# Performance work log

Hardware: AMD Instinct MI355X
Metric: run time of the kernel (lower is better)

## Reference

```python
import jax, jax.numpy as jnp
import numpy as np

B, C, H, W = 16, 192, 48, 48
D_STATE, DT_RANK, D_INNER, K = 16, 16, 288, 4


def setup_inputs() -> dict:
    key = jax.random.key(0)
    ks = jax.random.split(key, 8)
    g = lambda k, shape, scale: jax.random.normal(k, shape, jnp.float32) * scale
    # S4D-real style init: A_log = log(1..N)
    A_log = jnp.tile(jnp.log(jnp.arange(1.0, D_STATE + 1.0, dtype=jnp.float32)), (K, D_INNER, 1))
    return {
        "x": jax.random.normal(ks[0], (B, C, H, W), jnp.float32),
        "W_in": g(ks[1], (C, 2 * D_INNER), C ** -0.5),
        "conv_w": g(ks[2], (D_INNER, 1, 3, 3), 1.0 / 3.0),
        "conv_b": jnp.zeros((D_INNER,), jnp.float32),
        "x_proj_w": g(ks[3], (K, DT_RANK + 2 * D_STATE, D_INNER), D_INNER ** -0.5),
        "dt_w": g(ks[4], (K, D_INNER, DT_RANK), DT_RANK ** -0.5),
        "dt_b": g(ks[5], (K, D_INNER), 0.5) - 4.0,
        "A_log": A_log,
        "Ds": jnp.ones((K, D_INNER), jnp.float32),
        "ln_g": jnp.ones((D_INNER,), jnp.float32),
        "ln_b": jnp.zeros((D_INNER,), jnp.float32),
        "W_out": g(ks[6], (D_INNER, C), D_INNER ** -0.5),
        "bn_g": jnp.ones((C,), jnp.float32),
        "bn_b": jnp.zeros((C,), jnp.float32),
    }


def reference(x, W_in, conv_w, conv_b, x_proj_w, dt_w, dt_b, A_log, Ds,
              ln_g, ln_b, W_out, bn_g, bn_b):
    b, c, h, w = x.shape
    L = h * w
    # MambaBlock: NCHW -> NHWC, SS2D(v2), NHWC -> NCHW, BatchNorm2d
    xhwc = jnp.transpose(x, (0, 2, 3, 1))                        # (B,H,W,C)
    xz = xhwc @ W_in                                             # (B,H,W,2*Di)
    xc, z = jnp.split(xz, 2, axis=-1)
    # depthwise 3x3 conv + SiLU
    xc = jnp.transpose(xc, (0, 3, 1, 2))                         # (B,Di,H,W)
    xc = jax.lax.conv_general_dilated(
        xc, conv_w, (1, 1), ((1, 1), (1, 1)),
        dimension_numbers=('NCHW', 'OIHW', 'NCHW'),
        feature_group_count=D_INNER)
    xc = jax.nn.silu(xc + conv_b[None, :, None, None])
    # cross-scan: 4 directions (row-major, col-major, + reversals)
    x_hw = xc.reshape(b, D_INNER, L)
    x_wh = jnp.transpose(xc, (0, 1, 3, 2)).reshape(b, D_INNER, L)
    xs = jnp.stack([x_hw, x_wh], axis=1)
    xs = jnp.concatenate([xs, jnp.flip(xs, axis=-1)], axis=1)    # (B,K,Di,L)
    # input-dependent dt, B, C
    x_dbl = jnp.einsum('bkdl,kcd->bkcl', xs, x_proj_w)
    dts, Bmat, Cmat = jnp.split(x_dbl, [DT_RANK, DT_RANK + D_STATE], axis=2)
    dt = jnp.einsum('bkrl,kdr->bkdl', dts, dt_w)
    dt = jax.nn.softplus(dt + dt_b[None, :, :, None])            # (B,K,Di,L)
    A = -jnp.exp(A_log)                                          # (K,Di,N)
    # selective scan along L (sequential recurrence)
    us = jnp.transpose(xs, (3, 0, 1, 2))                         # (L,B,K,Di)
    dts_t = jnp.transpose(dt, (3, 0, 1, 2))
    Bs_t = jnp.transpose(Bmat, (3, 0, 1, 2))                     # (L,B,K,N)
    Cs_t = jnp.transpose(Cmat, (3, 0, 1, 2))

    def step(hst, inp):
        u_t, d_t, B_t, C_t = inp
        dA = jnp.exp(d_t[..., None] * A)                         # (B,K,Di,N)
        hst = dA * hst + (d_t * u_t)[..., None] * B_t[:, :, None, :]
        y_t = jnp.sum(hst * C_t[:, :, None, :], axis=-1)         # (B,K,Di)
        return hst, y_t

    h0 = jnp.zeros((b, K, D_INNER, D_STATE), xs.dtype)
    _, ys = jax.lax.scan(step, h0, (us, dts_t, Bs_t, Cs_t))
    ys = jnp.transpose(ys, (1, 2, 3, 0))                         # (B,K,Di,L)
    ys = ys + Ds[None, :, :, None] * xs                          # skip (D) term
    # cross-merge: undo flips / transpose and sum the 4 directions
    y = ys[:, 0] + jnp.flip(ys[:, 2], axis=-1)
    y_wh = ys[:, 1] + jnp.flip(ys[:, 3], axis=-1)                # col-major order
    y = y + jnp.transpose(y_wh.reshape(b, D_INNER, w, h), (0, 1, 3, 2)).reshape(b, D_INNER, L)
    y = jnp.transpose(y.reshape(b, D_INNER, h, w), (0, 2, 3, 1))  # (B,H,W,Di)
    # out_norm (LayerNorm over channels), gating, out projection
    mu = jnp.mean(y, axis=-1, keepdims=True)
    var = jnp.var(y, axis=-1, keepdims=True)
    y = (y - mu) * jax.lax.rsqrt(var + 1e-5) * ln_g + ln_b
    y = y * jax.nn.silu(z)
    out = jnp.transpose(y @ W_out, (0, 3, 1, 2))                 # (B,C,H,W)
    # BatchNorm2d (training-mode batch statistics)
    m = jnp.mean(out, axis=(0, 2, 3), keepdims=True)
    v = jnp.var(out, axis=(0, 2, 3), keepdims=True)
    out = (out - m) * jax.lax.rsqrt(v + 1e-5) * bn_g[None, :, None, None] + bn_b[None, :, None, None]
    return out
```

## Files before the change

kernel.cpp:

```cpp
#include <hip/hip_runtime.h>
#include <hip/hip_fp16.h>
#include <math.h>

#define BB 16
#define CC 192
#define LL 2304
#define DI 288
#define NS 16

typedef float f32x4 __attribute__((ext_vector_type(4)));
typedef short bf16x8 __attribute__((ext_vector_type(8)));

__device__ __forceinline__ short f2b(float f) {
  union { float f; unsigned u; } x; x.f = f;
  unsigned r = x.u + 0x7FFF + ((x.u >> 16) & 1);
  return (short)(r >> 16);
}

__device__ __forceinline__ float softplus_f(float v) {
  return v > 15.f ? v : __logf(1.f + __expf(v));
}

__device__ __forceinline__ int pos_of(int k, int t) {
  int tt = (k >= 2) ? (2303 - t) : t;
  if (k & 1) return (tt % 48) * 48 + tt / 48;
  return tt;
}
__device__ __forceinline__ int invpos(int k, int l) {
  int tt = (k & 1) ? (l % 48) * 48 + l / 48 : l;
  return (k >= 2) ? (2303 - tt) : tt;
}

__device__ __forceinline__ void pow_table(float E, float* P) {
  float p2 = E * E, p4 = p2 * p2, p8 = p4 * p4;
  P[0] = E;       P[1] = p2;      P[2] = p2 * E;  P[3] = p4;
  P[4] = p4 * E;  P[5] = p4 * p2; P[6] = p4 * P[2]; P[7] = p8;
  P[8] = p8 * E;  P[9] = p8 * p2; P[10] = p8 * P[2]; P[11] = p8 * p4;
  P[12] = p8 * P[4]; P[13] = p8 * P[5]; P[14] = p8 * P[6]; P[15] = p8 * p8;
}

__global__ __launch_bounds__(256) void k_wprep(const float* __restrict__ Win,
                                               const float* __restrict__ xpw,
                                               const float* __restrict__ Wout,
                                               short* __restrict__ winb,
                                               short* __restrict__ xpwb,
                                               short* __restrict__ woutb) {
  int i = blockIdx.x * 256 + threadIdx.x;
  if (i < 110592) {
    int j = i / 192, c = i % 192;
    winb[i] = f2b(Win[(size_t)c * 576 + j]);
  } else if (i < 165888) {
    int t = i - 110592;
    xpwb[t] = f2b(xpw[t]);
  } else {
    int t = i - 165888;
    int j = t / 288, d = t % 288;
    woutb[t] = f2b(Wout[(size_t)d * 192 + j]);
  }
}

__global__ __launch_bounds__(256) void k_check(const float* __restrict__ alog,
                                               int* __restrict__ flag) {
  __shared__ int ok;
  if (threadIdx.x == 0) ok = 1;
  __syncthreads();
  int bad = 0;
  for (int i = threadIdx.x; i < 4 * DI * NS; i += 256) {
    int n = i & 15;
    float t = __logf((float)(n + 1));
    if (fabsf(alog[i] - t) > 1e-5f) bad = 1;
  }
  if (bad) atomicAnd(&ok, 0);
  __syncthreads();
  if (threadIdx.x == 0) *flag = ok;
}

__global__ __launch_bounds__(256) void g_inproj(const float* __restrict__ x,
                                                const short* __restrict__ winb,
                                                float* __restrict__ xc,
                                                float* __restrict__ z) {
  __shared__ short As[64 * 200];
  __shared__ short Bs[48 * 200];
  int nt = blockIdx.x % 12, mt = blockIdx.x / 12;
  int b = mt / 36, l0 = (mt % 36) * 64;
  int j0 = nt * 48;
  int tid = threadIdx.x;
  for (int i = tid; i < 3072; i += 256) {
    int c = i >> 4, lq = i & 15;
    float4 v = *(const float4*)&x[((size_t)b * CC + c) * LL + l0 + lq * 4];
    As[(lq * 4 + 0) * 200 + c] = f2b(v.x);
    As[(lq * 4 + 1) * 200 + c] = f2b(v.y);
    As[(lq * 4 + 2) * 200 + c] = f2b(v.z);
    As[(lq * 4 + 3) * 200 + c] = f2b(v.w);
  }
  for (int i = tid; i < 1152; i += 256) {
    int n = i / 24, kq = i % 24;
    *(bf16x8*)&Bs[n * 200 + kq * 8] =
        *(const bf16x8*)&winb[(size_t)(j0 + n) * 192 + kq * 8];
  }
  __syncthreads();
  int w = tid >> 6, lane = tid & 63;
  int ln = lane & 15, q8 = (lane >> 4) * 8;
  int m0 = w * 16;
  f32x4 acc0 = {0.f, 0.f, 0.f, 0.f}, acc1 = acc0, acc2 = acc0;
#pragma unroll
  for (int kt = 0; kt < 6; ++kt) {
    bf16x8 a = *(bf16x8*)&As[(m0 + ln) * 200 + kt * 32 + q8];
    bf16x8 b0 = *(bf16x8*)&Bs[(0 * 16 + ln) * 200 + kt * 32 + q8];
    bf16x8 b1 = *(bf16x8*)&Bs[(1 * 16 + ln) * 200 + kt * 32 + q8];
    bf16x8 b2 = *(bf16x8*)&Bs[(2 * 16 + ln) * 200 + kt * 32 + q8];
    acc0 = __builtin_amdgcn_mfma_f32_16x16x32_bf16(a, b0, acc0, 0, 0, 0);
    acc1 = __builtin_amdgcn_mfma_f32_16x16x32_bf16(a, b1, acc1, 0, 0, 0);
    acc2 = __builtin_amdgcn_mfma_f32_16x16x32_bf16(a, b2, acc2, 0, 0, 0);
  }
  int mrow = m0 + (lane >> 4) * 4;
  if (nt < 6) {
#pragma unroll
    for (int r = 0; r < 4; ++r) {
      size_t rb = ((size_t)b * LL + l0 + mrow + r) * DI + j0;
      xc[rb + 0 * 16 + ln] = acc0[r];
      xc[rb + 1 * 16 + ln] = acc1[r];
      xc[rb + 2 * 16 + ln] = acc2[r];
    }
  } else {
    __syncthreads();
    float* Zs = (float*)As;
#pragma unroll
    for (int r = 0; r < 4; ++r) {
      int lm = mrow + r - 0;
      Zs[(0 * 16 + ln) * 66 + lm] = acc0[r];
      Zs[(1 * 16 + ln) * 66 + lm] = acc1[r];
      Zs[(2 * 16 + ln) * 66 + lm] = acc2[r];
    }
    __syncthreads();
    int j2base = j0 - DI;
    for (int i = tid; i < 768; i += 256) {
      int j = i >> 4, lq = i & 15;
      float4 v = make_float4(Zs[j * 66 + lq * 4 + 0], Zs[j * 66 + lq * 4 + 1],
                             Zs[j * 66 + lq * 4 + 2], Zs[j * 66 + lq * 4 + 3]);
      *(float4*)&z[((size_t)b * DI + j2base + j) * LL + l0 + lq * 4] = v;
    }
  }
}

__global__ __launch_bounds__(288) void k_conv2(const float* __restrict__ xc,
                                               const float* __restrict__ cw,
                                               const float* __restrict__ cb,
                                               float* __restrict__ co) {
  int b = blockIdx.x / 48, h = blockIdx.x % 48;
  int d = threadIdx.x;
  float wv[9];
#pragma unroll
  for (int j = 0; j < 9; ++j) wv[j] = cw[d * 9 + j];
  float bias = cb[d];
  bool hm = h > 0, hp = h < 47;
  const float* row0 = xc + ((size_t)b * LL + (h - 1) * 48) * DI + d;
  const float* row1 = xc + ((size_t)b * LL + h * 48) * DI + d;
  const float* row2 = xc + ((size_t)b * LL + (h + 1) * 48) * DI + d;
  float* op = co + ((size_t)b * LL + h * 48) * DI + d;
  float a0 = 0.f, a1 = 0.f, a2 = 0.f;
  float b0, b1, b2, c0, c1, c2;
  b0 = hm ? row0[0] : 0.f;
  b1 = row1[0];
  b2 = hp ? row2[0] : 0.f;
  for (int w = 0; w < 48; ++w) {
    if (w < 47) {
      int off = (w + 1) * DI;
      c0 = hm ? row0[off] : 0.f;
      c1 = row1[off];
      c2 = hp ? row2[off] : 0.f;
    } else {
      c0 = 0.f; c1 = 0.f; c2 = 0.f;
    }
    float acc = bias;
    acc = fmaf(a0, wv[0], acc); acc = fmaf(b0, wv[1], acc); acc = fmaf(c0, wv[2], acc);
    acc = fmaf(a1, wv[3], acc); acc = fmaf(b1, wv[4], acc); acc = fmaf(c1, wv[5], acc);
    acc = fmaf(a2, wv[6], acc); acc = fmaf(b2, wv[7], acc); acc = fmaf(c2, wv[8], acc);
    acc = acc / (1.f + __expf(-acc));
    op[w * DI] = acc;
    a0 = b0; a1 = b1; a2 = b2;
    b0 = c0; b1 = c1; b2 = c2;
  }
}

__global__ __launch_bounds__(256) void g_xdbl(const float* __restrict__ co,
                                              const short* __restrict__ xpwb,
                                              float* __restrict__ xd) {
  __shared__ short As[64 * 296];
  __shared__ short Bs[48 * 296];
  int nt = blockIdx.x % 4, mt = blockIdx.x / 4;
  int b = mt / 36, l0 = (mt % 36) * 64;
  int j0 = nt * 48;
  int tid = threadIdx.x;
  for (int i = tid; i < 2304; i += 256) {
    int m = i / 36, kq = i % 36;
    const float* src = &co[((size_t)b * LL + l0 + m) * DI + kq * 8];
    float4 f0 = *(const float4*)src;
    float4 f1 = *(const float4*)(src + 4);
    bf16x8 v;
    v[0] = f2b(f0.x); v[1] = f2b(f0.y); v[2] = f2b(f0.z); v[3] = f2b(f0.w);
    v[4] = f2b(f1.x); v[5] = f2b(f1.y); v[6] = f2b(f1.z); v[7] = f2b(f1.w);
    *(bf16x8*)&As[m * 296 + kq * 8] = v;
  }
  for (int i = tid; i < 1728; i += 256) {
    int n = i / 36, kq = i % 36;
    *(bf16x8*)&Bs[n * 296 + kq * 8] =
        *(const bf16x8*)&xpwb[(size_t)(j0 + n) * 288 + kq * 8];
  }
  __syncthreads();
  int w = tid >> 6, lane = tid & 63;
  int ln = lane & 15, q8 = (lane >> 4) * 8;
  int m0 = w * 16;
  f32x4 acc0 = {0.f, 0.f, 0.f, 0.f}, acc1 = acc0, acc2 = acc0;
#pragma unroll
  for (int kt = 0; kt < 9; ++kt) {
    bf16x8 a = *(bf16x8*)&As[(m0 + ln) * 296 + kt * 32 + q8];
    bf16x8 b0 = *(bf16x8*)&Bs[(0 * 16 + ln) * 296 + kt * 32 + q8];
    bf16x8 b1 = *(bf16x8*)&Bs[(1 * 16 + ln) * 296 + kt * 32 + q8];
    bf16x8 b2 = *(bf16x8*)&Bs[(2 * 16 + ln) * 296 + kt * 32 + q8];
    acc0 = __builtin_amdgcn_mfma_f32_16x16x32_bf16(a, b0, acc0, 0, 0, 0);
    acc1 = __builtin_amdgcn_mfma_f32_16x16x32_bf16(a, b1, acc1, 0, 0, 0);
    acc2 = __builtin_amdgcn_mfma_f32_16x16x32_bf16(a, b2, acc2, 0, 0, 0);
  }
  int mrow = m0 + (lane >> 4) * 4;
#pragma unroll
  for (int r = 0; r < 4; ++r) {
    size_t rb = (((size_t)b * 4 + nt) * LL + l0 + mrow + r) * 48;
    xd[rb + 0 * 16 + ln] = acc0[r];
    xd[rb + 1 * 16 + ln] = acc1[r];
    xd[rb + 2 * 16 + ln] = acc2[r];
  }
}

__global__ __launch_bounds__(288) void g_dt(const float* __restrict__ xd,
                                            const float* __restrict__ dtw,
                                            const float* __restrict__ dtb,
                                            __half* __restrict__ dth) {
  int blk = blockIdx.x;
  int lc = blk % 72, bk = blk / 72;
  int k = bk & 3;
  int d = threadIdx.x;
  float w_dt[16];
#pragma unroll
  for (int r4 = 0; r4 < 4; ++r4) {
    float4 t4 = *(const float4*)&dtw[((size_t)k * DI + d) * 16 + r4 * 4];
    w_dt[r4 * 4 + 0] = t4.x; w_dt[r4 * 4 + 1] = t4.y;
    w_dt[r4 * 4 + 2] = t4.z; w_dt[r4 * 4 + 3] = t4.w;
  }
  float bias = dtb[k * DI + d];
  const float* __restrict__ xb = xd + (size_t)bk * LL * 48;
  __half* __restrict__ Eb = dth + (size_t)bk * LL * DI;
#pragma unroll 2
  for (int j = 0; j < 32; ++j) {
    int l = lc * 32 + j;
    const float* __restrict__ xr = xb + (size_t)l * 48;
    float4 v0 = *(const float4*)(xr + 0);
    float4 v1 = *(const float4*)(xr + 4);
    float4 v2 = *(const float4*)(xr + 8);
    float4 v3 = *(const float4*)(xr + 12);
    float a0 = fmaf(v0.x, w_dt[0], bias);
    float a1 = v0.y * w_dt[1];
    float a2 = v0.z * w_dt[2];
    float a3 = v0.w * w_dt[3];
    a0 = fmaf(v1.x, w_dt[4], a0); a1 = fmaf(v1.y, w_dt[5], a1);
    a2 = fmaf(v1.z, w_dt[6], a2); a3 = fmaf(v1.w, w_dt[7], a3);
    a0 = fmaf(v2.x, w_dt[8], a0); a1 = fmaf(v2.y, w_dt[9], a1);
    a2 = fmaf(v2.z, w_dt[10], a2); a3 = fmaf(v2.w, w_dt[11], a3);
    a0 = fmaf(v3.x, w_dt[12], a0); a1 = fmaf(v3.y, w_dt[13], a1);
    a2 = fmaf(v3.z, w_dt[14], a2); a3 = fmaf(v3.w, w_dt[15], a3);
    float v = (a0 + a1) + (a2 + a3);
    float dt = v > 15.f ? v : __logf(1.f + __expf(v));
    int t = invpos(k, l);
    Eb[(size_t)t * DI + d] = __float2half(dt);
  }
}

template <int SCHT, bool USE_E>
__global__ __launch_bounds__(288) void k_pass1(const float* __restrict__ co,
                                               const float* __restrict__ xd,
                                               const float* __restrict__ dtw,
                                               const float* __restrict__ dtb,
                                               const float* __restrict__ alog,
                                               const int* __restrict__ flag,
                                               const __half* __restrict__ dth,
                                               float* __restrict__ HL,
                                               float* __restrict__ Sd) {
  constexpr int TCHT = LL / SCHT;
  int blk = blockIdx.x;
  int s = blk % SCHT, k = (blk / SCHT) & 3, b = blk / (SCHT * 4);
  int d = threadIdx.x;
  float w_dt[16];
  float bias = 0.f;
  if constexpr (!USE_E) {
#pragma unroll
    for (int r4 = 0; r4 < 4; ++r4) {
      float4 t4 = *(const float4*)&dtw[((size_t)k * DI + d) * 16 + r4 * 4];
      w_dt[r4 * 4 + 0] = t4.x; w_dt[r4 * 4 + 1] = t4.y;
      w_dt[r4 * 4 + 2] = t4.z; w_dt[r4 * 4 + 3] = t4.w;
    }
    bias = dtb[k * DI + d];
  }
  float h[16];
#pragma unroll
  for (int n = 0; n < 16; ++n) h[n] = 0.f;
  const float* __restrict__ xb = xd + ((size_t)b * 4 + k) * LL * 48;
  const float* __restrict__ cb_ = co + (size_t)b * LL * DI;
  const __half* __restrict__ Eb = dth + ((size_t)b * 4 + k) * LL * DI;
  int fast = *flag;
  size_t base = ((size_t)((b * 4 + k) * SCHT + s) * DI + d) * 16;
  size_t sbase = ((size_t)((b * 4 + k) * SCHT + s) * DI + d);
  float S = 0.f;
  if (fast) {
    for (int i = 0; i < TCHT; ++i) {
      int t = s * TCHT + i;
      int l = __builtin_amdgcn_readfirstlane(pos_of(k, t));
      const float* __restrict__ xr = xb + (size_t)l * 48;
      float4 q0 = *(const float4*)(xr + 16);
      float4 q1 = *(const float4*)(xr + 20);
      float4 q2 = *(const float4*)(xr + 24);
      float4 q3 = *(const float4*)(xr + 28);
      float u = cb_[(size_t)l * DI + d];
      float E, dt;
      if constexpr (USE_E) {
        dt = __half2float(Eb[(size_t)t * DI + d]);
        E = __expf(-dt);
      } else {
        float4 v0 = *(const float4*)(xr + 0);
        float4 v1 = *(const float4*)(xr + 4);
        float4 v2 = *(const float4*)(xr + 8);
        float4 v3 = *(const float4*)(xr + 12);
        float a0 = fmaf(v0.x, w_dt[0], bias), a1 = v0.y * w_dt[1];
        float a2 = v0.z * w_dt[2], a3 = v0.w * w_dt[3];
        a0 = fmaf(v1.x, w_dt[4], a0); a1 = fmaf(v1.y, w_dt[5], a1);
        a2 = fmaf(v1.z, w_dt[6], a2); a3 = fmaf(v1.w, w_dt[7], a3);
        a0 = fmaf(v2.x, w_dt[8], a0); a1 = fmaf(v2.y, w_dt[9], a1);
        a2 = fmaf(v2.z, w_dt[10], a2); a3 = fmaf(v2.w, w_dt[11], a3);
        a0 = fmaf(v3.x, w_dt[12], a0); a1 = fmaf(v3.y, w_dt[13], a1);
        a2 = fmaf(v3.z, w_dt[14], a2); a3 = fmaf(v3.w, w_dt[15], a3);
        float v = (a0 + a1) + (a2 + a3);
        float ev = __expf(v);
        E = __builtin_amdgcn_rcpf(1.f + ev);
        dt = v > 15.f ? v : __logf(1.f + ev);
      }
      float xv = dt * u;
      S += dt;
      float P[16];
      pow_table(E, P);
      float Bv[16] = {q0.x, q0.y, q0.z, q0.w, q1.x, q1.y, q1.z, q1.w,
                      q2.x, q2.y, q2.z, q2.w, q3.x, q3.y, q3.z, q3.w};
#pragma unroll
      for (int n = 0; n < 16; ++n) h[n] = fmaf(P[n], h[n], xv * Bv[n]);
    }
  } else {
    float A[16];
#pragma unroll
    for (int n = 0; n < 16; ++n) A[n] = -__expf(alog[((size_t)k * DI + d) * 16 + n]);
    for (int i = 0; i < TCHT; ++i) {
      int t = s * TCHT + i;
      int l = __builtin_amdgcn_readfirstlane(pos_of(k, t));
      const float* __restrict__ xr = xb + (size_t)l * 48;
      float4 q0 = *(const float4*)(xr + 16);
      float4 q1 = *(const float4*)(xr + 20);
      float4 q2 = *(const float4*)(xr + 24);
      float4 q3 = *(const float4*)(xr + 28);
      float u = cb_[(size_t)l * DI + d];
      float dt;
      if constexpr (USE_E) {
        dt = __half2float(Eb[(size_t)t * DI + d]);
      } else {
        float a0 = bias, a1 = 0.f, a2 = 0.f, a3 = 0.f;
#pragma unroll
        for (int r = 0; r < 4; ++r) {
          a0 = fmaf(xr[r * 4 + 0], w_dt[r * 4 + 0], a0);
          a1 = fmaf(xr[r * 4 + 1], w_dt[r * 4 + 1], a1);
          a2 = fmaf(xr[r * 4 + 2], w_dt[r * 4 + 2], a2);
          a3 = fmaf(xr[r * 4 + 3], w_dt[r * 4 + 3], a3);
        }
        dt = softplus_f((a0 + a1) + (a2 + a3));
      }
      float xv = dt * u;
      S += dt;
      float Bv[16] = {q0.x, q0.y, q0.z, q0.w, q1.x, q1.y, q1.z, q1.w,
                      q2.x, q2.y, q2.z, q2.w, q3.x, q3.y, q3.z, q3.w};
#pragma unroll
      for (int n = 0; n < 16; ++n) {
        float dA = __expf(dt * A[n]);
        h[n] = fmaf(dA, h[n], xv * Bv[n]);
      }
    }
  }
  Sd[sbase] = S;
#pragma unroll
  for (int n = 0; n < 16; ++n) HL[base + n] = h[n];
}

template <int SCHT>
__global__ __launch_bounds__(256) void k_stitch(float* __restrict__ HL,
                                                const float* __restrict__ Sd,
                                                const float* __restrict__ alog,
                                                const int* __restrict__ flag) {
  int idx = blockIdx.x * 256 + threadIdx.x;
  if (idx >= 64 * DI) return;
  int d = idx % DI, bk = idx / DI;
  int k = bk & 3;
  int fast = *flag;
  float A[16];
  if (!fast) {
#pragma unroll
    for (int n = 0; n < 16; ++n) A[n] = -__expf(alog[((size_t)k * DI + d) * 16 + n]);
  }
  float h[16];
#pragma unroll
  for (int n = 0; n < 16; ++n) h[n] = 0.f;
  for (int s = 0; s < SCHT; ++s) {
    size_t base = ((size_t)(bk * SCHT + s) * DI + d) * 16;
    float S = Sd[(size_t)(bk * SCHT + s) * DI + d];
    float Q[16];
    if (fast) {
      pow_table(__expf(-S), Q);
    } else {
#pragma unroll
      for (int n = 0; n < 16; ++n) Q[n] = __expf(A[n] * S);
    }
#pragma unroll
    for (int n = 0; n < 16; ++n) {
      float hl = HL[base + n];
      HL[base + n] = h[n];
      h[n] = fmaf(Q[n], h[n], hl);
    }
  }
}

template <int SCHT, bool USE_E>
__global__ __launch_bounds__(288) void k_pass2(const float* __restrict__ co,
                                               const float* __restrict__ xd,
                                               const float* __restrict__ dtw,
                                               const float* __restrict__ dtb,
                                               const float* __restrict__ alog,
                                               const int* __restrict__ flag,
                                               const __half* __restrict__ dth,
                                               const float* __restrict__ Hin,
                                               float* __restrict__ ym) {
  constexpr int TCHT = LL / SCHT;
  int blk = blockIdx.x;
  int s = blk % SCHT, k = (blk / SCHT) & 3, b = blk / (SCHT * 4);
  int d = threadIdx.x;
  float w_dt[16];
  float bias = 0.f;
  if constexpr (!USE_E) {
#pragma unroll
    for (int r4 = 0; r4 < 4; ++r4) {
      float4 t4 = *(const float4*)&dtw[((size_t)k * DI + d) * 16 + r4 * 4];
      w_dt[r4 * 4 + 0] = t4.x; w_dt[r4 * 4 + 1] = t4.y;
      w_dt[r4 * 4 + 2] = t4.z; w_dt[r4 * 4 + 3] = t4.w;
    }
    bias = dtb[k * DI + d];
  }
  size_t base = ((size_t)((b * 4 + k) * SCHT + s) * DI + d) * 16;
  float h[16];
#pragma unroll
  for (int n = 0; n < 16; ++n) h[n] = Hin[base + n];
  const float* __restrict__ xb = xd + ((size_t)b * 4 + k) * LL * 48;
  const float* __restrict__ cb_ = co + (size_t)b * LL * DI;
  const __half* __restrict__ Eb = dth + ((size_t)b * 4 + k) * LL * DI;
  float* __restrict__ yb = ym + (size_t)b * LL * DI;
  int fast = *flag;
  if (fast) {
    for (int i = 0; i < TCHT; ++i) {
      int t = s * TCHT + i;
      int l = __builtin_amdgcn_readfirstlane(pos_of(k, t));
      const float* __restrict__ xr = xb + (size_t)l * 48;
      float4 q0 = *(const float4*)(xr + 16);
      float4 q1 = *(const float4*)(xr + 20);
      float4 q2 = *(const float4*)(xr + 24);
      float4 q3 = *(const float4*)(xr + 28);
      float4 c0 = *(const float4*)(xr + 32);
      float4 c1 = *(const float4*)(xr + 36);
      float4 c2 = *(const float4*)(xr + 40);
      float4 c3 = *(const float4*)(xr + 44);
      float u = cb_[(size_t)l * DI + d];
      float E, dt;
      if constexpr (USE_E) {
        dt = __half2float(Eb[(size_t)t * DI + d]);
        E = __expf(-dt);
      } else {
        float4 v0 = *(const float4*)(xr + 0);
        float4 v1 = *(const float4*)(xr + 4);
        float4 v2 = *(const float4*)(xr + 8);
        float4 v3 = *(const float4*)(xr + 12);
        float a0 = fmaf(v0.x, w_dt[0], bias), a1 = v0.y * w_dt[1];
        float a2 = v0.z * w_dt[2], a3 = v0.w * w_dt[3];
        a0 = fmaf(v1.x, w_dt[4], a0); a1 = fmaf(v1.y, w_dt[5], a1);
        a2 = fmaf(v1.z, w_dt[6], a2); a3 = fmaf(v1.w, w_dt[7], a3);
        a0 = fmaf(v2.x, w_dt[8], a0); a1 = fmaf(v2.y, w_dt[9], a1);
        a2 = fmaf(v2.z, w_dt[10], a2); a3 = fmaf(v2.w, w_dt[11], a3);
        a0 = fmaf(v3.x, w_dt[12], a0); a1 = fmaf(v3.y, w_dt[13], a1);
        a2 = fmaf(v3.z, w_dt[14], a2); a3 = fmaf(v3.w, w_dt[15], a3);
        float v = (a0 + a1) + (a2 + a3);
        float ev = __expf(v);
        E = __builtin_amdgcn_rcpf(1.f + ev);
        dt = v > 15.f ? v : __logf(1.f + ev);
      }
      float xv = dt * u;
      float P[16];
      pow_table(E, P);
      float Bv[16] = {q0.x, q0.y, q0.z, q0.w, q1.x, q1.y, q1.z, q1.w,
                      q2.x, q2.y, q2.z, q2.w, q3.x, q3.y, q3.z, q3.w};
      float Cv[16] = {c0.x, c0.y, c0.z, c0.w, c1.x, c1.y, c1.z, c1.w,
                      c2.x, c2.y, c2.z, c2.w, c3.x, c3.y, c3.z, c3.w};
      float y0 = 0.f, y1 = 0.f, y2 = 0.f, y3 = 0.f;
#pragma unroll
      for (int n = 0; n < 16; n += 4) {
        h[n + 0] = fmaf(P[n + 0], h[n + 0], xv * Bv[n + 0]);
        h[n + 1] = fmaf(P[n + 1], h[n + 1], xv * Bv[n + 1]);
        h[n + 2] = fmaf(P[n + 2], h[n + 2], xv * Bv[n + 2]);
        h[n + 3] = fmaf(P[n + 3], h[n + 3], xv * Bv[n + 3]);
        y0 = fmaf(h[n + 0], Cv[n + 0], y0);
        y1 = fmaf(h[n + 1], Cv[n + 1], y1);
        y2 = fmaf(h[n + 2], Cv[n + 2], y2);
        y3 = fmaf(h[n + 3], Cv[n + 3], y3);
      }
      atomicAdd(&yb[(size_t)l * DI + d], (y0 + y1) + (y2 + y3));
    }
  } else {
    float A[16];
#pragma unroll
    for (int n = 0; n < 16; ++n) A[n] = -__expf(alog[((size_t)k * DI + d) * 16 + n]);
    for (int i = 0; i < TCHT; ++i) {
      int t = s * TCHT + i;
      int l = __builtin_amdgcn_readfirstlane(pos_of(k, t));
      const float* __restrict__ xr = xb + (size_t)l * 48;
      float4 q0 = *(const float4*)(xr + 16);
      float4 q1 = *(const float4*)(xr + 20);
      float4 q2 = *(const float4*)(xr + 24);
      float4 q3 = *(const float4*)(xr + 28);
      float4 c0 = *(const float4*)(xr + 32);
      float4 c1 = *(const float4*)(xr + 36);
      float4 c2 = *(const float4*)(xr + 40);
      float4 c3 = *(const float4*)(xr + 44);
      float u = cb_[(size_t)l * DI + d];
      float dt;
      if constexpr (USE_E) {
        dt = __half2float(Eb[(size_t)t * DI + d]);
      } else {
        float a0 = bias, a1 = 0.f, a2 = 0.f, a3 = 0.f;
#pragma unroll
        for (int r = 0; r < 4; ++r) {
          a0 = fmaf(xr[r * 4 + 0], w_dt[r * 4 + 0], a0);
          a1 = fmaf(xr[r * 4 + 1], w_dt[r * 4 + 1], a1);
          a2 = fmaf(xr[r * 4 + 2], w_dt[r * 4 + 2], a2);
          a3 = fmaf(xr[r * 4 + 3], w_dt[r * 4 + 3], a3);
        }
        dt = softplus_f((a0 + a1) + (a2 + a3));
      }
      float xv = dt * u;
      float Bv[16] = {q0.x, q0.y, q0.z, q0.w, q1.x, q1.y, q1.z, q1.w,
                      q2.x, q2.y, q2.z, q2.w, q3.x, q3.y, q3.z, q3.w};
      float Cv[16] = {c0.x, c0.y, c0.z, c0.w, c1.x, c1.y, c1.z, c1.w,
                      c2.x, c2.y, c2.z, c2.w, c3.x, c3.y, c3.z, c3.w};
      float y = 0.f;
#pragma unroll
      for (int n = 0; n < 16; ++n) {
        float dA = __expf(dt * A[n]);
        h[n] = fmaf(dA, h[n], xv * Bv[n]);
        y = fmaf(h[n], Cv[n], y);
      }
      atomicAdd(&yb[(size_t)l * DI + d], y);
    }
  }
}

__global__ __launch_bounds__(256) void k_ln(const float* __restrict__ ym,
                                            const float* __restrict__ co,
                                            const float* __restrict__ z,
                                            const float* __restrict__ Ds,
                                            const float* __restrict__ lng,
                                            const float* __restrict__ lnb,
                                            float* __restrict__ Yl) {
  __shared__ float As[DI * 33];
  __shared__ float red[512];
  __shared__ float mus[32], rss[32];
  int b = blockIdx.x / 72;
  int l0 = (blockIdx.x % 72) * 32;
  for (int i = threadIdx.x; i < DI * 32; i += 256) {
    int l = i / DI, d = i % DI;
    float sds = Ds[d] + Ds[DI + d] + Ds[2 * DI + d] + Ds[3 * DI + d];
    size_t off = ((size_t)b * LL + l0 + l) * DI + d;
    As[d * 33 + l] = ym[off] + sds * co[off];
  }
  __syncthreads();
  int l = threadIdx.x & 31;
  int p = threadIdx.x >> 5;
  float s1 = 0.f, s2 = 0.f;
  for (int d = p; d < DI; d += 8) {
    float v = As[d * 33 + l];
    s1 += v; s2 += v * v;
  }
  red[p * 32 + l] = s1;
  red[256 + p * 32 + l] = s2;
  __syncthreads();
  if (threadIdx.x < 32) {
    float su = 0.f, sq = 0.f;
#pragma unroll
    for (int q = 0; q < 8; ++q) { su += red[q * 32 + l]; sq += red[256 + q * 32 + l]; }
    float mu = su * (1.f / 288.f);
    float var = sq * (1.f / 288.f) - mu * mu;
    mus[l] = mu;
    rss[l] = rsqrtf(var + 1e-5f);
  }
  __syncthreads();
  {
    float mu = mus[l], rs = rss[l];
    for (int d = p; d < DI; d += 8) {
      float v = (As[d * 33 + l] - mu) * rs * lng[d] + lnb[d];
      float zv = z[((size_t)b * DI + d) * LL + l0 + l];
      v *= zv / (1.f + __expf(-zv));
      As[d * 33 + l] = v;
    }
  }
  __syncthreads();
  for (int i = threadIdx.x; i < DI * 32; i += 256) {
    int ll = i / DI, d = i % DI;
    Yl[((size_t)b * LL + l0 + ll) * DI + d] = As[d * 33 + ll];
  }
}

__global__ __launch_bounds__(256) void g_outproj(const float* __restrict__ Yl,
                                                 const short* __restrict__ woutb,
                                                 float* __restrict__ out,
                                                 float* __restrict__ bnsum,
                                                 float* __restrict__ bnsq) {
  __shared__ short As[64 * 296];
  __shared__ short Bs[48 * 296];
  int nt = blockIdx.x % 4, mt = blockIdx.x / 4;
  int b = mt / 36, l0 = (mt % 36) * 64;
  int j0 = nt * 48;
  int tid = threadIdx.x;
  for (int i = tid; i < 2304; i += 256) {
    int m = i / 36, kq = i % 36;
    const float* src = &Yl[((size_t)b * LL + l0 + m) * DI + kq * 8];
    float4 f0 = *(const float4*)src;
    float4 f1 = *(const float4*)(src + 4);
    bf16x8 v;
    v[0] = f2b(f0.x); v[1] = f2b(f0.y); v[2] = f2b(f0.z); v[3] = f2b(f0.w);
    v[4] = f2b(f1.x); v[5] = f2b(f1.y); v[6] = f2b(f1.z); v[7] = f2b(f1.w);
    *(bf16x8*)&As[m * 296 + kq * 8] = v;
  }
  for (int i = tid; i < 1728; i += 256) {
    int n = i / 36, kq = i % 36;
    *(bf16x8*)&Bs[n * 296 + kq * 8] =
        *(const bf16x8*)&woutb[(size_t)(j0 + n) * 288 + kq * 8];
  }
  __syncthreads();
  int w = tid >> 6, lane = tid & 63;
  int ln = lane & 15, q8 = (lane >> 4) * 8;
  int m0 = w * 16;
  f32x4 acc0 = {0.f, 0.f, 0.f, 0.f}, acc1 = acc0, acc2 = acc0;
#pragma unroll
  for (int kt = 0; kt < 9; ++kt) {
    bf16x8 a = *(bf16x8*)&As[(m0 + ln) * 296 + kt * 32 + q8];
    bf16x8 b0 = *(bf16x8*)&Bs[(0 * 16 + ln) * 296 + kt * 32 + q8];
    bf16x8 b1 = *(bf16x8*)&Bs[(1 * 16 + ln) * 296 + kt * 32 + q8];
    bf16x8 b2 = *(bf16x8*)&Bs[(2 * 16 + ln) * 296 + kt * 32 + q8];
    acc0 = __builtin_amdgcn_mfma_f32_16x16x32_bf16(a, b0, acc0, 0, 0, 0);
    acc1 = __builtin_amdgcn_mfma_f32_16x16x32_bf16(a, b1, acc1, 0, 0, 0);
    acc2 = __builtin_amdgcn_mfma_f32_16x16x32_bf16(a, b2, acc2, 0, 0, 0);
  }
  __syncthreads();
  float* Zs = (float*)As;
  int lm = m0 + (lane >> 4) * 4;
#pragma unroll
  for (int r = 0; r < 4; ++r) {
    Zs[(0 * 16 + ln) * 66 + lm + r] = acc0[r];
    Zs[(1 * 16 + ln) * 66 + lm + r] = acc1[r];
    Zs[(2 * 16 + ln) * 66 + lm + r] = acc2[r];
  }
  __syncthreads();
  for (int i = tid; i < 768; i += 256) {
    int j = i >> 4, lq = i & 15;
    float4 v = make_float4(Zs[j * 66 + lq * 4 + 0], Zs[j * 66 + lq * 4 + 1],
                           Zs[j * 66 + lq * 4 + 2], Zs[j * 66 + lq * 4 + 3]);
    *(float4*)&out[((size_t)b * CC + j0 + j) * LL + l0 + lq * 4] = v;
  }
  if (tid < 48) {
    float s1 = 0.f, s2 = 0.f;
#pragma unroll 8
    for (int l = 0; l < 64; ++l) {
      float v = Zs[tid * 66 + l];
      s1 += v; s2 += v * v;
    }
    atomicAdd(&bnsum[j0 + tid], s1);
    atomicAdd(&bnsq[j0 + tid], s2);
  }
}

__global__ __launch_bounds__(256) void k_bnfin(float* __restrict__ out,
                                               const float* __restrict__ bnsum,
                                               const float* __restrict__ bnsq,
                                               const float* __restrict__ bg,
                                               const float* __restrict__ bb) {
  int idx = blockIdx.x * 256 + threadIdx.x;
  int c = (idx / LL) % CC;
  float mean = bnsum[c] * (1.f / 36864.f);
  float var = bnsq[c] * (1.f / 36864.f) - mean * mean;
  float sc = bg[c] * rsqrtf(var + 1e-5f);
  out[idx] = (out[idx] - mean) * sc + bb[c];
}

extern "C" void kernel_launch(void* const* d_in, const int* in_sizes, int n_in,
                              void* d_out, int out_size, void* d_ws, size_t ws_size,
                              hipStream_t stream) {
  (void)in_sizes; (void)n_in; (void)out_size;
  const float* x    = (const float*)d_in[0];
  const float* Win  = (const float*)d_in[1];
  const float* cw   = (const float*)d_in[2];
  const float* cbb  = (const float*)d_in[3];
  const float* xpw  = (const float*)d_in[4];
  const float* dtw  = (const float*)d_in[5];
  const float* dtb  = (const float*)d_in[6];
  const float* alog = (const float*)d_in[7];
  const float* Ds   = (const float*)d_in[8];
  const float* lng  = (const float*)d_in[9];
  const float* lnb  = (const float*)d_in[10];
  const float* Wout = (const float*)d_in[11];
  const float* bg   = (const float*)d_in[12];
  const float* bb   = (const float*)d_in[13];
  float* out = (float*)d_out;

  const size_t NXC = 10616832, NXD = 7077888;
  const size_t NWB = 110592;
  const size_t NE  = 42467328;
  const size_t REH = NE / 2;
  auto hlN = [](int sch) { return (size_t)64 * sch * DI * 16; };
  auto sdN = [](int sch) { return (size_t)64 * sch * DI; };
  auto needE = [&](int sch) {
    return (3 * NXC + NWB + NXD + REH + hlN(sch) + sdN(sch) + 1024) * 4;
  };
  auto needN = [&](int sch) {
    return (3 * NXC + NWB + NXD + hlN(sch) + sdN(sch) + 1024) * 4;
  };
  bool useE; int sch;
  if (ws_size >= needE(32))      { useE = true;  sch = 32; }
  else if (ws_size >= needE(16)) { useE = true;  sch = 16; }
  else if (ws_size >= needN(32)) { useE = false; sch = 32; }
  else                           { useE = false; sch = 16; }

  float* ws = (float*)d_ws;
  float* z   = ws;
  float* A1  = z + NXC;
  float* co  = A1 + NXC;
  float* wbF = co + NXC;
  float* xd  = wbF + NWB;
  float* R   = xd + NXD;
  short* winb  = (short*)wbF;
  short* xpwb  = (short*)(wbF + 55296);
  short* woutb = (short*)(wbF + 55296 + 27648);
  float *xc, *ym, *tail;
  __half* dth = nullptr;
  if (useE) {
    xc = R;
    ym = A1;
    dth = (__half*)R;
    tail = R + REH;
  } else {
    xc = A1; ym = A1;
    tail = R;
  }
  float* HL = tail;
  float* Sd = HL + hlN(sch);
  float* bnsum = Sd + sdN(sch);
  float* bnsq  = bnsum + 192;
  int*   flag  = (int*)(bnsq + 192);
  float* Yl = xd;

  k_wprep<<<864, 256, 0, stream>>>(Win, xpw, Wout, winb, xpwb, woutb);
  k_check<<<1, 256, 0, stream>>>(alog, flag);
  g_inproj<<<6912, 256, 0, stream>>>(x, winb, xc, z);
  k_conv2<<<768, 288, 0, stream>>>(xc, cw, cbb, co);
  hipMemsetAsync(ym, 0, NXC * 4, stream);
  hipMemsetAsync(bnsum, 0, 2 * 192 * 4, stream);
  g_xdbl<<<2304, 256, 0, stream>>>(co, xpwb, xd);
  if (useE) g_dt<<<4608, 288, 0, stream>>>(xd, dtw, dtb, dth);
  if (useE && sch == 32) {
    k_pass1<32, true><<<2048, 288, 0, stream>>>(co, xd, dtw, dtb, alog, flag, dth, HL, Sd);
    k_stitch<32><<<72, 256, 0, stream>>>(HL, Sd, alog, flag);
    k_pass2<32, true><<<2048, 288, 0, stream>>>(co, xd, dtw, dtb, alog, flag, dth, HL, ym);
  } else if (useE) {
    k_pass1<16, true><<<1024, 288, 0, stream>>>(co, xd, dtw, dtb, alog, flag, dth, HL, Sd);
    k_stitch<16><<<72, 256, 0, stream>>>(HL, Sd, alog, flag);
    k_pass2<16, true><<<1024, 288, 0, stream>>>(co, xd, dtw, dtb, alog, flag, dth, HL, ym);
  } else if (sch == 32) {
    k_pass1<32, false><<<2048, 288, 0, stream>>>(co, xd, dtw, dtb, alog, flag, dth, HL, Sd);
    k_stitch<32><<<72, 256, 0, stream>>>(HL, Sd, alog, flag);
    k_pass2<32, false><<<2048, 288, 0, stream>>>(co, xd, dtw, dtb, alog, flag, dth, HL, ym);
  } else {
    k_pass1<16, false><<<1024, 288, 0, stream>>>(co, xd, dtw, dtb, alog, flag, dth, HL, Sd);
    k_stitch<16><<<72, 256, 0, stream>>>(HL, Sd, alog, flag);
    k_pass2<16, false><<<1024, 288, 0, stream>>>(co, xd, dtw, dtb, alog, flag, dth, HL, ym);
  }
  k_ln<<<1152, 256, 0, stream>>>(ym, co, z, Ds, lng, lnb, Yl);
  g_outproj<<<2304, 256, 0, stream>>>(Yl, woutb, out, bnsum, bnsq);
  k_bnfin<<<27648, 256, 0, stream>>>(out, bnsum, bnsq, bg, bb);
}
```

Measured before the change: 706.4 us.

## Stage B/C scan rows in double-buffered LDS and prefetch next-step inputs

In the USE_E fast path of both scan passes, each block now cooperatively loads the B (and C) vectors for groups of 18 timesteps into a double-buffered shared-memory tile, prefetching the next group while the current one is processed. Per-step u and dt values are also software-prefetched one step ahead in registers. This replaces the per-thread broadcast global loads on the serial critical path with LDS reads and hides global latency. In exchange it adds block-wide barriers per group and extra LDS traffic, and it assumes TCHT is a multiple of 18.

```diff
diff --git a/kernel.cpp b/kernel.cpp
--- a/kernel.cpp
+++ b/kernel.cpp
@@ -286,9 +286,12 @@
                                                float* __restrict__ HL,
                                                float* __restrict__ Sd) {
   constexpr int TCHT = LL / SCHT;
+  constexpr int G = 18;
+  __shared__ float ro[2][G * 16];
   int blk = blockIdx.x;
   int s = blk % SCHT, k = (blk / SCHT) & 3, b = blk / (SCHT * 4);
   int d = threadIdx.x;
+  int tid = threadIdx.x;
   float w_dt[16];
   float bias = 0.f;
   if constexpr (!USE_E) {
@@ -310,7 +313,52 @@
   size_t base = ((size_t)((b * 4 + k) * SCHT + s) * DI + d) * 16;
   size_t sbase = ((size_t)((b * 4 + k) * SCHT + s) * DI + d);
   float S = 0.f;
-  if (fast) {
+  if (fast && USE_E) {
+    int t0 = s * TCHT, tend = t0 + TCHT;
+    {
+      int i = tid >> 4, j = tid & 15;
+      int lg = pos_of(k, t0 + i);
+      ro[0][tid] = xb[(size_t)lg * 48 + 16 + j];
+    }
+    int lc = __builtin_amdgcn_readfirstlane(pos_of(k, t0));
+    float u = cb_[(size_t)lc * DI + d];
+    __half dh = Eb[(size_t)t0 * DI + d];
+    __syncthreads();
+    for (int g = 0; g < TCHT / G; ++g) {
+      int buf = g & 1;
+      if (g + 1 < TCHT / G) {
+        int i = tid >> 4, j = tid & 15;
+        int lg = pos_of(k, t0 + (g + 1) * G + i);
+        ro[buf ^ 1][tid] = xb[(size_t)lg * 48 + 16 + j];
+      }
+      for (int il = 0; il < G; ++il) {
+        int t = t0 + g * G + il;
+        float un = u; __half dhn = dh;
+        if (t + 1 < tend) {
+          int ln_ = __builtin_amdgcn_readfirstlane(pos_of(k, t + 1));
+          un = cb_[(size_t)ln_ * DI + d];
+          dhn = Eb[(size_t)(t + 1) * DI + d];
+        }
+        float dt = __half2float(dh);
+        float E = __expf(-dt);
+        float xv = dt * u;
+        S += dt;
+        float P[16];
+        pow_table(E, P);
+        const float* rp = &ro[buf][il * 16];
+        float4 r0 = *(const float4*)(rp + 0);
+        float4 r1 = *(const float4*)(rp + 4);
+        float4 r2 = *(const float4*)(rp + 8);
+        float4 r3 = *(const float4*)(rp + 12);
+        float Bv[16] = {r0.x, r0.y, r0.z, r0.w, r1.x, r1.y, r1.z, r1.w,
+                        r2.x, r2.y, r2.z, r2.w, r3.x, r3.y, r3.z, r3.w};
+#pragma unroll
+        for (int n = 0; n < 16; ++n) h[n] = fmaf(P[n], h[n], xv * Bv[n]);
+        u = un; dh = dhn;
+      }
+      __syncthreads();
+    }
+  } else if (fast) {
     for (int i = 0; i < TCHT; ++i) {
       int t = s * TCHT + i;
       int l = __builtin_amdgcn_readfirstlane(pos_of(k, t));
@@ -320,28 +368,22 @@
       float4 q2 = *(const float4*)(xr + 24);
       float4 q3 = *(const float4*)(xr + 28);
       float u = cb_[(size_t)l * DI + d];
-      float E, dt;
-      if constexpr (USE_E) {
-        dt = __half2float(Eb[(size_t)t * DI + d]);
-        E = __expf(-dt);
-      } else {
-        float4 v0 = *(const float4*)(xr + 0);
-        float4 v1 = *(const float4*)(xr + 4);
-        float4 v2 = *(const float4*)(xr + 8);
-        float4 v3 = *(const float4*)(xr + 12);
-        float a0 = fmaf(v0.x, w_dt[0], bias), a1 = v0.y * w_dt[1];
-        float a2 = v0.z * w_dt[2], a3 = v0.w * w_dt[3];
-        a0 = fmaf(v1.x, w_dt[4], a0); a1 = fmaf(v1.y, w_dt[5], a1);
-        a2 = fmaf(v1.z, w_dt[6], a2); a3 = fmaf(v1.w, w_dt[7], a3);
-        a0 = fmaf(v2.x, w_dt[8], a0); a1 = fmaf(v2.y, w_dt[9], a1);
-        a2 = fmaf(v2.z, w_dt[10], a2); a3 = fmaf(v2.w, w_dt[11], a3);
-        a0 = fmaf(v3.x, w_dt[12], a0); a1 = fmaf(v3.y, w_dt[13], a1);
-        a2 = fmaf(v3.z, w_dt[14], a2); a3 = fmaf(v3.w, w_dt[15], a3);
-        float v = (a0 + a1) + (a2 + a3);
-        float ev = __expf(v);
-        E = __builtin_amdgcn_rcpf(1.f + ev);
-        dt = v > 15.f ? v : __logf(1.f + ev);
-      }
+      float4 v0 = *(const float4*)(xr + 0);
+      float4 v1 = *(const float4*)(xr + 4);
+      float4 v2 = *(const float4*)(xr + 8);
+      float4 v3 = *(const float4*)(xr + 12);
+      float a0 = fmaf(v0.x, w_dt[0], bias), a1 = v0.y * w_dt[1];
+      float a2 = v0.z * w_dt[2], a3 = v0.w * w_dt[3];
+      a0 = fmaf(v1.x, w_dt[4], a0); a1 = fmaf(v1.y, w_dt[5], a1);
+      a2 = fmaf(v1.z, w_dt[6], a2); a3 = fmaf(v1.w, w_dt[7], a3);
+      a0 = fmaf(v2.x, w_dt[8], a0); a1 = fmaf(v2.y, w_dt[9], a1);
+      a2 = fmaf(v2.z, w_dt[10], a2); a3 = fmaf(v2.w, w_dt[11], a3);
+      a0 = fmaf(v3.x, w_dt[12], a0); a1 = fmaf(v3.y, w_dt[13], a1);
+      a2 = fmaf(v3.z, w_dt[14], a2); a3 = fmaf(v3.w, w_dt[15], a3);
+      float v = (a0 + a1) + (a2 + a3);
+      float ev = __expf(v);
+      float E = __builtin_amdgcn_rcpf(1.f + ev);
+      float dt = v > 15.f ? v : __logf(1.f + ev);
       float xv = dt * u;
       S += dt;
       float P[16];
@@ -442,9 +484,12 @@
                                                const float* __restrict__ Hin,
                                                float* __restrict__ ym) {
   constexpr int TCHT = LL / SCHT;
+  constexpr int G = 18;
+  __shared__ float ro[2][G * 32];
   int blk = blockIdx.x;
   int s = blk % SCHT, k = (blk / SCHT) & 3, b = blk / (SCHT * 4);
   int d = threadIdx.x;
+  int tid = threadIdx.x;
   float w_dt[16];
   float bias = 0.f;
   if constexpr (!USE_E) {
@@ -465,7 +510,75 @@
   const __half* __restrict__ Eb = dth + ((size_t)b * 4 + k) * LL * DI;
   float* __restrict__ yb = ym + (size_t)b * LL * DI;
   int fast = *flag;
-  if (fast) {
+  if (fast && USE_E) {
+    int t0 = s * TCHT, tend = t0 + TCHT;
+    {
+      int f0 = tid, i = f0 >> 5, j = f0 & 31;
+      int lg = pos_of(k, t0 + i);
+      ro[0][f0] = xb[(size_t)lg * 48 + 16 + j];
+      int f1 = tid + 288; i = f1 >> 5; j = f1 & 31;
+      lg = pos_of(k, t0 + i);
+      ro[0][f1] = xb[(size_t)lg * 48 + 16 + j];
+    }
+    int lc = __builtin_amdgcn_readfirstlane(pos_of(k, t0));
+    float u = cb_[(size_t)lc * DI + d];
+    __half dh = Eb[(size_t)t0 * DI + d];
+    __syncthreads();
+    for (int g = 0; g < TCHT / G; ++g) {
+      int buf = g & 1;
+      if (g + 1 < TCHT / G) {
+        int tg = t0 + (g + 1) * G;
+        int f0 = tid, i = f0 >> 5, j = f0 & 31;
+        int lg = pos_of(k, tg + i);
+        ro[buf ^ 1][f0] = xb[(size_t)lg * 48 + 16 + j];
+        int f1 = tid + 288; i = f1 >> 5; j = f1 & 31;
+        lg = pos_of(k, tg + i);
+        ro[buf ^ 1][f1] = xb[(size_t)lg * 48 + 16 + j];
+      }
+      for (int il = 0; il < G; ++il) {
+        int t = t0 + g * G + il;
+        int lnx = lc; float un = u; __half dhn = dh;
+        if (t + 1 < tend) {
+          lnx = __builtin_amdgcn_readfirstlane(pos_of(k, t + 1));
+          un = cb_[(size_t)lnx * DI + d];
+          dhn = Eb[(size_t)(t + 1) * DI + d];
+        }
+        float dt = __half2float(dh);
+        float E = __expf(-dt);
+        float xv = dt * u;
+        float P[16];
+        pow_table(E, P);
+        const float* rp = &ro[buf][il * 32];
+        float4 r0 = *(const float4*)(rp + 0);
+        float4 r1 = *(const float4*)(rp + 4);
+        float4 r2 = *(const float4*)(rp + 8);
+        float4 r3 = *(const float4*)(rp + 12);
+        float4 r4 = *(const float4*)(rp + 16);
+        float4 r5 = *(const float4*)(rp + 20);
+        float4 r6 = *(const float4*)(rp + 24);
+        float4 r7 = *(const float4*)(rp + 28);
+        float Bv[16] = {r0.x, r0.y, r0.z, r0.w, r1.x, r1.y, r1.z, r1.w,
+                        r2.x, r2.y, r2.z, r2.w, r3.x, r3.y, r3.z, r3.w};
+        float Cv[16] = {r4.x, r4.y, r4.z, r4.w, r5.x, r5.y, r5.z, r5.w,
+                        r6.x, r6.y, r6.z, r6.w, r7.x, r7.y, r7.z, r7.w};
+        float y0 = 0.f, y1 = 0.f, y2 = 0.f, y3 = 0.f;
+#pragma unroll
+        for (int n = 0; n < 16; n += 4) {
+          h[n + 0] = fmaf(P[n + 0], h[n + 0], xv * Bv[n + 0]);
+          h[n + 1] = fmaf(P[n + 1], h[n + 1], xv * Bv[n + 1]);
+          h[n + 2] = fmaf(P[n + 2], h[n + 2], xv * Bv[n + 2]);
+          h[n + 3] = fmaf(P[n + 3], h[n + 3], xv * Bv[n + 3]);
+          y0 = fmaf(h[n + 0], Cv[n + 0], y0);
+          y1 = fmaf(h[n + 1], Cv[n + 1], y1);
+          y2 = fmaf(h[n + 2], Cv[n + 2], y2);
+          y3 = fmaf(h[n + 3], Cv[n + 3], y3);
+        }
+        atomicAdd(&yb[(size_t)lc * DI + d], (y0 + y1) + (y2 + y3));
+        lc = lnx; u = un; dh = dhn;
+      }
+      __syncthreads();
+    }
+  } else if (fast) {
     for (int i = 0; i < TCHT; ++i) {
       int t = s * TCHT + i;
       int l = __builtin_amdgcn_readfirstlane(pos_of(k, t));
@@ -479,28 +592,22 @@
       float4 c2 = *(const float4*)(xr + 40);
       float4 c3 = *(const float4*)(xr + 44);
       float u = cb_[(size_t)l * DI + d];
-      float E, dt;
-      if constexpr (USE_E) {
-        dt = __half2float(Eb[(size_t)t * DI + d]);
-        E = __expf(-dt);
-      } else {
-        float4 v0 = *(const float4*)(xr + 0);
-        float4 v1 = *(const float4*)(xr + 4);
-        float4 v2 = *(const float4*)(xr + 8);
-        float4 v3 = *(const float4*)(xr + 12);
-        float a0 = fmaf(v0.x, w_dt[0], bias), a1 = v0.y * w_dt[1];
-        float a2 = v0.z * w_dt[2], a3 = v0.w * w_dt[3];
-        a0 = fmaf(v1.x, w_dt[4], a0); a1 = fmaf(v1.y, w_dt[5], a1);
-        a2 = fmaf(v1.z, w_dt[6], a2); a3 = fmaf(v1.w, w_dt[7], a3);
-        a0 = fmaf(v2.x, w_dt[8], a0); a1 = fmaf(v2.y, w_dt[9], a1);
-        a2 = fmaf(v2.z, w_dt[10], a2); a3 = fmaf(v2.w, w_dt[11], a3);
-        a0 = fmaf(v3.x, w_dt[12], a0); a1 = fmaf(v3.y, w_dt[13], a1);
-        a2 = fmaf(v3.z, w_dt[14], a2); a3 = fmaf(v3.w, w_dt[15], a3);
-        float v = (a0 + a1) + (a2 + a3);
-        float ev = __expf(v);
-        E = __builtin_amdgcn_rcpf(1.f + ev);
-        dt = v > 15.f ? v : __logf(1.f + ev);
-      }
+      float4 v0 = *(const float4*)(xr + 0);
+      float4 v1 = *(const float4*)(xr + 4);
+      float4 v2 = *(const float4*)(xr + 8);
+      float4 v3 = *(const float4*)(xr + 12);
+      float a0 = fmaf(v0.x, w_dt[0], bias), a1 = v0.y * w_dt[1];
+      float a2 = v0.z * w_dt[2], a3 = v0.w * w_dt[3];
+      a0 = fmaf(v1.x, w_dt[4], a0); a1 = fmaf(v1.y, w_dt[5], a1);
+      a2 = fmaf(v1.z, w_dt[6], a2); a3 = fmaf(v1.w, w_dt[7], a3);
+      a0 = fmaf(v2.x, w_dt[8], a0); a1 = fmaf(v2.y, w_dt[9], a1);
+      a2 = fmaf(v2.z, w_dt[10], a2); a3 = fmaf(v2.w, w_dt[11], a3);
+      a0 = fmaf(v3.x, w_dt[12], a0); a1 = fmaf(v3.y, w_dt[13], a1);
+      a2 = fmaf(v3.z, w_dt[14], a2); a3 = fmaf(v3.w, w_dt[15], a3);
+      float v = (a0 + a1) + (a2 + a3);
+      float ev = __expf(v);
+      float E = __builtin_amdgcn_rcpf(1.f + ev);
+      float dt = v > 15.f ? v : __logf(1.f + ev);
       float xv = dt * u;
       float P[16];
       pow_table(E, P);
```

Result: slower. 733.3 us (+3.8%).
